# Performance work log

Hardware: AMD Instinct MI355X
Metric: run time of the kernel (lower is better)

The kernel has to match this reference:

```python
import jax, jax.numpy as jnp
import numpy as np

B, T, A, H, E = 256, 64, 32, 512, 32


def setup_inputs() -> dict:
    key = jax.random.key(0)
    ks = jax.random.split(key, 8)
    return {
        "actions": jax.random.normal(ks[0], (B, T, A), dtype=jnp.float32),
        "timesteps": jax.random.randint(ks[1], (B,), 0, 1000, dtype=jnp.int32),
        "cat_ids": jax.random.randint(ks[2], (B,), 0, E, dtype=jnp.int32),
        "W1": 0.02 * jax.random.normal(ks[3], (E, A, H), dtype=jnp.float32),
        "b1": jnp.zeros((E, H), dtype=jnp.float32),
        "W2": 0.02 * jax.random.normal(ks[4], (E, 2 * H, H), dtype=jnp.float32),
        "b2": jnp.zeros((E, H), dtype=jnp.float32),
        "W3": 0.02 * jax.random.normal(ks[5], (E, H, H), dtype=jnp.float32),
        "b3": jnp.zeros((E, H), dtype=jnp.float32),
    }


def _cat_linear(x, cat_ids, W, b):
    # per-sample weight gather + bmm, faithful to torch W[cat_ids]; bmm
    return jnp.einsum("btd,bdh->bth", x, W[cat_ids]) + b[cat_ids][:, None, :]


def _sinusoidal(timesteps_bt, dim):
    half = dim // 2
    exponent = -jnp.arange(half, dtype=jnp.float32) * (jnp.log(jnp.float32(10000.0)) / half)
    freqs = timesteps_bt[..., None] * jnp.exp(exponent)  # (B,T,half)
    return jnp.concatenate([jnp.sin(freqs), jnp.cos(freqs)], axis=-1)


def _swish(x):
    return x * jax.nn.sigmoid(x)


def reference(actions, timesteps, cat_ids, W1, b1, W2, b2, W3, b3):
    Bb, Tt, _ = actions.shape
    t_bt = jnp.broadcast_to(timesteps.astype(jnp.float32)[:, None], (Bb, Tt))
    a_emb = _cat_linear(actions, cat_ids, W1, b1)                     # (B,T,H)
    tau_emb = _sinusoidal(t_bt, a_emb.shape[-1]).astype(a_emb.dtype)  # (B,T,H)
    x = jnp.concatenate([a_emb, tau_emb], axis=-1)                    # (B,T,2H)
    x = _swish(_cat_linear(x, cat_ids, W2, b2))
    return _cat_linear(x, cat_ids, W3, b3)
```

## Files before the change

kernel.cpp:

```cpp
#include <hip/hip_runtime.h>
#include <hip/hip_bf16.h>

#define NB 256
#define NT 64
#define NA 32
#define NH 512
#define NE 32
#define MAXTILES 144

typedef short short8 __attribute__((ext_vector_type(8)));
typedef unsigned short ushort8v __attribute__((ext_vector_type(8)));
typedef float f32x4 __attribute__((ext_vector_type(4)));

__device__ __forceinline__ unsigned short f2bf(float f) {
  unsigned int u = __float_as_uint(f);
  u += 0x7FFFu + ((u >> 16) & 1u);
  return (unsigned short)(u >> 16);
}

__device__ __forceinline__ void gl2lds16(const void* g, void* l) {
  __builtin_amdgcn_global_load_lds(
      (const __attribute__((address_space(1))) unsigned int*)g,
      (__attribute__((address_space(3))) unsigned int*)l, 16, 0, 0);
}

__device__ __forceinline__ ushort8v cvt8(float4 a, float4 b) {
  ushort8v t;
  t[0] = f2bf(a.x); t[1] = f2bf(a.y); t[2] = f2bf(a.z); t[3] = f2bf(a.w);
  t[4] = f2bf(b.x); t[5] = f2bf(b.y); t[6] = f2bf(b.z); t[7] = f2bf(b.w);
  return t;
}

__device__ __forceinline__ void pfld(float2 (&pf)[8], const float* __restrict__ base,
                                     int c, int tid) {
#pragma unroll
  for (int j = 0; j < 8; j++) {
    int u = j * 256 + tid;
    int kk = u >> 7, cc = u & 127;
    pf[j] = *(const float2*)(base + (size_t)(c * 16 + kk) * NH + cc * 2);
  }
}

template <bool BIASDOT>
__device__ __forceinline__ void stream_block(
    const float* __restrict__ Wbase, float* S, unsigned short* Bs,
    const unsigned short* As, const float* b1S, int tid, int w, int lrow,
    int kq, f32x4 (&acc)[2][4], float& bacc) {
  float2 pf[2][8];
  pfld(pf[0], Wbase, 0, tid);
  pfld(pf[1], Wbase, 1, tid);
#pragma unroll 2
  for (int c = 0; c < 32; c++) {
    const int cur = c & 1;
    __syncthreads();
#pragma unroll
    for (int j = 0; j < 8; j++) {
      int u = j * 256 + tid;
      int kk = u >> 7, cc = u & 127;
      *(float2*)(&S[kk * 260 + cc * 2]) = pf[cur][j];
    }
    if (c + 2 < 32) pfld(pf[cur], Wbase, c + 2, tid);
    __syncthreads();
    {
      int n = tid;
      ushort8v pk0, pk1;
#pragma unroll
      for (int kk = 0; kk < 8; kk++) {
        float sv = S[kk * 260 + n];
        pk0[kk] = f2bf(sv);
        if (BIASDOT) bacc += sv * b1S[c * 16 + kk];
      }
#pragma unroll
      for (int kk = 8; kk < 16; kk++) {
        float sv = S[kk * 260 + n];
        pk1[kk - 8] = f2bf(sv);
        if (BIASDOT) bacc += sv * b1S[c * 16 + kk];
      }
      *(ushort8v*)(&Bs[n * 40 + cur * 16]) = pk0;
      *(ushort8v*)(&Bs[n * 40 + cur * 16 + 8]) = pk1;
    }
    if (cur) {
      __syncthreads();
      int w2i = c >> 1;
      short8 bf[4], af[2];
#pragma unroll
      for (int ni = 0; ni < 4; ni++)
        bf[ni] = *(short8*)(&Bs[(w * 64 + ni * 16 + lrow) * 40 + kq * 8]);
#pragma unroll
      for (int mi = 0; mi < 2; mi++) {
        int a = mi * 16 + lrow;
        int ck = w2i * 4 + kq;
        af[mi] = *(short8*)(&As[a * 512 + ((ck ^ (a & 7)) << 3)]);
      }
#pragma unroll
      for (int mi = 0; mi < 2; mi++)
#pragma unroll
        for (int ni = 0; ni < 4; ni++)
          acc[mi][ni] = __builtin_amdgcn_mfma_f32_16x16x32_bf16(
              af[mi], bf[ni], acc[mi][ni], 0, 0, 0);
    }
  }
}

__global__ __launch_bounds__(256) void wp2_kernel(
    const float* __restrict__ W1, const float* __restrict__ b1,
    const float* __restrict__ W2, const float* __restrict__ b2,
    const float* __restrict__ W3, const int* __restrict__ timesteps,
    const int* __restrict__ cat, unsigned short* __restrict__ Wt12,
    float* __restrict__ bias2G, float* __restrict__ tvec,
    unsigned short* __restrict__ Wt3, int* __restrict__ tiles,
    int* __restrict__ ntiles_out) {
  __shared__ __align__(16) unsigned char smem[71936];
  int tid = threadIdx.x;
  int bx = blockIdx.x;

  if (bx >= 128 && bx < 640) {
    float* S2 = (float*)smem;
    unsigned short* Bt = (unsigned short*)(smem + 33280);
    int id = bx - 128;
    int e = id >> 4, kb = (id >> 1) & 7, nh = id & 1;
    int kt = kb * 64, nt = nh * 256;
#pragma unroll
    for (int h = 0; h < 2; h++) {
      if (h) __syncthreads();
#pragma unroll
      for (int j = 0; j < 16; j++) {
        int u = j * 256 + tid;
        int kk = u >> 7, cc = u & 127;
        float2 v = *(const float2*)(W3 + ((size_t)e * 512 + kt + h * 32 + kk) * NH +
                                    nt + cc * 2);
        *(float2*)(&S2[kk * 260 + cc * 2]) = v;
      }
      __syncthreads();
      {
        int n = tid;
#pragma unroll
        for (int q = 0; q < 4; q++) {
          ushort8v pk;
#pragma unroll
          for (int jj = 0; jj < 8; jj++)
            pk[jj] = f2bf(S2[(q * 8 + jj) * 260 + n]);
          *(ushort8v*)(&Bt[n * 72 + h * 32 + q * 8]) = pk;
        }
      }
    }
    __syncthreads();
    {
      int n = tid;
      unsigned short* dst = Wt3 + (((size_t)e * 8 + kb) * 512 + nt + n) * 64;
#pragma unroll
      for (int q = 0; q < 8; q++)
        *(ushort8v*)(dst + q * 8) = *(ushort8v*)(&Bt[n * 72 + q * 8]);
    }
    return;
  }

  if (bx == 640) {
    int* cnt = (int*)smem;
    int* off = cnt + 32;
    int* cur = off + 32;
    int* order = cur + 32;
    if (tid < NE) cnt[tid] = 0;
    __syncthreads();
    int e = cat[tid];
    atomicAdd(&cnt[e], 1);
    __syncthreads();
    if (tid == 0) {
      int s = 0;
      for (int i = 0; i < NE; i++) { off[i] = s; cur[i] = s; s += cnt[i]; }
    }
    __syncthreads();
    int p = atomicAdd(&cur[e], 1);
    order[p] = tid;
    __syncthreads();
    if (tid == 0) {
      int nt = 0;
      for (int i = 0; i < NE; i++) {
        for (int j = 0; j < cnt[i]; j += 2) {
          tiles[3 * nt + 0] = i;
          tiles[3 * nt + 1] = order[off[i] + j];
          tiles[3 * nt + 2] = (j + 1 < cnt[i]) ? order[off[i] + j + 1] : -1;
          nt++;
        }
      }
      *ntiles_out = nt;
    }
    return;
  }

  float* S           = (float*)smem;
  unsigned short* Bs = (unsigned short*)(smem + 16640);
  unsigned short* As = (unsigned short*)(smem + 37120);
  float* b1S         = (float*)(smem + 69888);
  int* list          = (int*)(smem + 69888);
  int* pcnt          = (int*)(smem + 70912);

  int w = tid >> 6, l = tid & 63;
  int lrow = l & 15, kq = l >> 4;

  if (bx < 64) {
    int e = bx >> 1, nh = bx & 1;
    const float* Wbase = W2 + ((size_t)e << 19) + nh * 256;
    const float* W1e = W1 + ((size_t)e << 14);
    {
      float2 v = *(const float2*)(b1 + (size_t)e * NH + tid * 2);
      *(float2*)(&b1S[tid * 2]) = v;
    }
    {
      int a = tid >> 3, seg = tid & 7;
#pragma unroll
      for (int p = 0; p < 8; p++) {
        const float* src = W1e + (size_t)a * NH + p * 64 + seg * 8;
        float4 v0 = *(const float4*)src;
        float4 v1 = *(const float4*)(src + 4);
        int ch = p * 8 + seg;
        *(ushort8v*)(&As[a * 512 + ((ch ^ (a & 7)) << 3)]) = cvt8(v0, v1);
      }
    }
    f32x4 acc[2][4];
#pragma unroll
    for (int mi = 0; mi < 2; mi++)
#pragma unroll
      for (int ni = 0; ni < 4; ni++) acc[mi][ni] = (f32x4){0.f, 0.f, 0.f, 0.f};
    float bacc = 0.f;
    stream_block<true>(Wbase, S, Bs, As, b1S, tid, w, lrow, kq, acc, bacc);

    __syncthreads();
    unsigned short* Sb = Bs;
#pragma unroll
    for (int mi = 0; mi < 2; mi++)
#pragma unroll
      for (int ni = 0; ni < 4; ni++)
#pragma unroll
        for (int r = 0; r < 4; r++)
          Sb[(w * 64 + ni * 16 + lrow) * 40 + mi * 16 + kq * 4 + r] =
              f2bf(acc[mi][ni][r]);
    bias2G[(size_t)e * NH + nh * 256 + tid] =
        bacc + b2[(size_t)e * NH + nh * 256 + tid];
    __syncthreads();
    {
      int n = tid;
      unsigned short* dst = Wt12 + ((size_t)e * NH + nh * 256 + n) * NA;
#pragma unroll
      for (int q = 0; q < 4; q++)
        *(ushort8v*)(dst + q * 8) = *(ushort8v*)(&Sb[n * 40 + q * 8]);
    }
    return;
  }

  {
    int id = bx - 64;
    int e = id >> 1, nh = id & 1;
    const float* Wbase = W2 + ((size_t)e << 19) + ((size_t)512 * NH) + nh * 256;
    if (tid == 0) *pcnt = 0;
    __syncthreads();
    if (cat[tid] == e) { int p = atomicAdd(pcnt, 1); list[p] = tid; }
    __syncthreads();
    int c = *pcnt;
    if (c == 0) return;
    const float kLog = 0.035977893400931146f;

    for (int sg = 0; sg * 32 < c; sg++) {
      if (sg) __syncthreads();
      {
        int a = tid >> 3, seg = tid & 7;
        int si = sg * 32 + a;
        float tv = (si < c) ? (float)timesteps[list[si]] : 0.f;
#pragma unroll
        for (int p = 0; p < 8; p++) {
          ushort8v pk;
#pragma unroll
          for (int q = 0; q < 8; q++) {
            int k = p * 64 + seg * 8 + q;
            float f = expf(-(float)(k & 255) * kLog);
            float ang = tv * f;
            pk[q] = f2bf((k < 256) ? sinf(ang) : cosf(ang));
          }
          int ch = p * 8 + seg;
          *(ushort8v*)(&As[a * 512 + ((ch ^ (a & 7)) << 3)]) = pk;
        }
      }
      f32x4 acc[2][4];
#pragma unroll
      for (int mi = 0; mi < 2; mi++)
#pragma unroll
        for (int ni = 0; ni < 4; ni++) acc[mi][ni] = (f32x4){0.f, 0.f, 0.f, 0.f};
      float dummy = 0.f;
      stream_block<false>(Wbase, S, Bs, As, nullptr, tid, w, lrow, kq, acc, dummy);
#pragma unroll
      for (int mi = 0; mi < 2; mi++)
#pragma unroll
        for (int ni = 0; ni < 4; ni++)
#pragma unroll
          for (int r = 0; r < 4; r++) {
            int a = mi * 16 + kq * 4 + r;
            int si = sg * 32 + a;
            if (si < c)
              tvec[(size_t)list[si] * NH + nh * 256 + w * 64 + ni * 16 + lrow] =
                  acc[mi][ni][r];
          }
    }
  }
}

__global__ __launch_bounds__(256) void gemmh_kernel(
    const float* __restrict__ actions, const unsigned short* __restrict__ Wt12,
    const float* __restrict__ tvec, const float* __restrict__ bias2,
    const int* __restrict__ cat_ids, unsigned short* __restrict__ Hb) {
  __shared__ __align__(16) unsigned char smem[16384 + 5120 + 33792];
  unsigned short* Ws = (unsigned short*)smem;
  unsigned short* As = (unsigned short*)(smem + 16384);
  unsigned short* Ts = (unsigned short*)(smem + 16384 + 5120);

  int b = blockIdx.y, h = blockIdx.x;
  int tid = threadIdx.x;
  int e = cat_ids[b];

  {
    const unsigned short* wsrc = Wt12 + ((size_t)e * NH + h * 256) * NA;
#pragma unroll
    for (int j = 0; j < 4; j++) {
      int u = j * 256 + tid;
      int n = u >> 2, p = u & 3;
      int ch = p ^ ((n >> 1) & 3);
      gl2lds16(wsrc + (size_t)n * NA + ch * 8,
               Ws + (size_t)(j * 256 + (tid & 448)) * 8);
    }
  }
  {
    int row = tid >> 2, seg = tid & 3;
    const float* src = actions + (size_t)(b * NT + row) * NA + seg * 8;
    float4 v0 = *(const float4*)(src);
    float4 v1 = *(const float4*)(src + 4);
    *(ushort8v*)(&As[row * 40 + seg * 8]) = cvt8(v0, v1);
  }
  __syncthreads();

  int w = tid >> 6, l = tid & 63;
  int lrow = l & 15, kq = l >> 4;
  short8 af = *(short8*)(&As[(w * 16 + lrow) * 40 + kq * 8]);
  f32x4 zero = {0.f, 0.f, 0.f, 0.f};
  f32x4 acc[16];
#pragma unroll
  for (int ni = 0; ni < 16; ni++) {
    int nn = ni * 16 + lrow;
    int p = kq ^ ((nn >> 1) & 3);
    short8 bfv = *(short8*)(&Ws[nn * 32 + p * 8]);
    acc[ni] = __builtin_amdgcn_mfma_f32_16x16x32_bf16(af, bfv, zero, 0, 0, 0);
  }
#pragma unroll
  for (int ni = 0; ni < 16; ni++) {
    int colL = ni * 16 + lrow;
    float bv = tvec[(size_t)b * NH + h * 256 + colL] +
               bias2[(size_t)e * NH + h * 256 + colL];
#pragma unroll
    for (int r = 0; r < 4; r++) {
      int row = w * 16 + kq * 4 + r;
      float v = acc[ni][r] + bv;
      v = v / (1.0f + __expf(-v));
      Ts[row * 264 + colL] = f2bf(v);
    }
  }
  __syncthreads();
#pragma unroll
  for (int i = 0; i < 8; i++) {
    int u = i * 256 + tid;
    int t = u >> 5, c4 = u & 31;
    uint4 v = *(uint4*)(&Ts[t * 264 + c4 * 8]);
    *(uint4*)(Hb + ((size_t)(b * NT + t)) * NH + h * 256 + c4 * 8) = v;
  }
}

template <int KTOT, bool HASTAU, bool SWISH, bool OUT_BF16>
__global__ __launch_bounds__(256) void gemm2_kernel(
    const unsigned short* __restrict__ Xa, const unsigned short* __restrict__ Xt,
    const unsigned short* __restrict__ Wt, const float* __restrict__ bias,
    void* __restrict__ Yv, const int* __restrict__ tiles,
    const int* __restrict__ pntiles) {
  __shared__ __align__(16) unsigned char smem[49152];

  int ti = blockIdx.y;
  if (ti >= *pntiles) return;
  int n0 = blockIdx.x * 64;
  int e = tiles[3 * ti], s0 = tiles[3 * ti + 1], s1 = tiles[3 * ti + 2];
  int s1v = (s1 < 0) ? s0 : s1;

  int tid = threadIdx.x;
  int l = tid & 63;
  int wr = (tid >> 7), wc = (tid >> 6) & 1;
  int lrow = l & 15, kq = l >> 4;

  constexpr int NIT = KTOT / 64;

  auto stage = [&](int it, int buf) {
    unsigned short* As = (unsigned short*)(smem + buf * 24576);
    unsigned short* Bs = (unsigned short*)(smem + buf * 24576 + 16384);
    int k0 = it * 64;
#pragma unroll
    for (int j = 0; j < 4; j++) {
      int u = j * 256 + tid;
      int row = u >> 3, p = u & 7;
      int ch = p ^ (row & 7);
      int kk = k0 + ch * 8;
      int s = (row < 64) ? s0 : s1v;
      const unsigned short* src;
      if (HASTAU && kk >= 512)
        src = Xt + (size_t)s * NH + (kk - 512);
      else
        src = Xa + ((size_t)(s * NT + (row & 63))) * NH + kk;
      gl2lds16(src, As + (size_t)(j * 256 + (tid & 448)) * 8);
    }
#pragma unroll
    for (int j = 0; j < 2; j++) {
      int u = j * 256 + tid;
      int n = u >> 3, p = u & 7;
      int ch = p ^ (n & 7);
      gl2lds16(Wt + (((size_t)e * 8 + it) * 512 + n0 + n) * 64 + ch * 8,
               Bs + (size_t)(j * 256 + (tid & 448)) * 8);
    }
  };

  f32x4 acc[4][2];
#pragma unroll
  for (int mi = 0; mi < 4; mi++)
#pragma unroll
    for (int ni = 0; ni < 2; ni++) acc[mi][ni] = (f32x4){0.f, 0.f, 0.f, 0.f};

  stage(0, 0);
  stage(1, 1);

  for (int t = 0; t < NIT; t++) {
    int cur = t & 1;
    unsigned short* As = (unsigned short*)(smem + cur * 24576);
    unsigned short* Bs = (unsigned short*)(smem + cur * 24576 + 16384);

    if (t + 1 < NIT) {
      asm volatile("s_waitcnt vmcnt(6)" ::: "memory");
    } else {
      asm volatile("s_waitcnt vmcnt(0)" ::: "memory");
    }
    __builtin_amdgcn_sched_barrier(0);
    __builtin_amdgcn_s_barrier();
    __builtin_amdgcn_sched_barrier(0);

    short8 afr[2][4], bfr[2][2];
#pragma unroll
    for (int s2 = 0; s2 < 2; s2++) {
#pragma unroll
      for (int mi = 0; mi < 4; mi++) {
        int row = wr * 64 + mi * 16 + lrow;
        int p = (s2 * 4 + kq) ^ (row & 7);
        afr[s2][mi] = *(short8*)(&As[row * 64 + p * 8]);
      }
#pragma unroll
      for (int ni = 0; ni < 2; ni++) {
        int n = wc * 32 + ni * 16 + lrow;
        int p = (s2 * 4 + kq) ^ (n & 7);
        bfr[s2][ni] = *(short8*)(&Bs[n * 64 + p * 8]);
      }
    }
    asm volatile("s_waitcnt lgkmcnt(0)" ::: "memory");
    __builtin_amdgcn_sched_barrier(0);
    __builtin_amdgcn_s_barrier();
    __builtin_amdgcn_sched_barrier(0);

    if (t + 2 < NIT) stage(t + 2, cur);

#pragma unroll
    for (int s2 = 0; s2 < 2; s2++)
#pragma unroll
      for (int mi = 0; mi < 4; mi++)
#pragma unroll
        for (int ni = 0; ni < 2; ni++)
          acc[mi][ni] = __builtin_amdgcn_mfma_f32_16x16x32_bf16(
              afr[s2][mi], bfr[s2][ni], acc[mi][ni], 0, 0, 0);
  }
  __syncthreads();

#pragma unroll
  for (int ni = 0; ni < 2; ni++) {
    int colL = wc * 32 + ni * 16 + lrow;
    float bv = bias[(size_t)e * NH + n0 + colL];
#pragma unroll
    for (int mi = 0; mi < 4; mi++) {
#pragma unroll
      for (int r = 0; r < 4; r++) {
        int row = wr * 64 + mi * 16 + kq * 4 + r;
        float v = acc[mi][ni][r] + bv;
        if (SWISH) v = v / (1.0f + __expf(-v));
        if (OUT_BF16)
          ((unsigned short*)smem)[row * 80 + colL] = f2bf(v);
        else
          ((float*)smem)[row * 68 + colL] = v;
      }
    }
  }
  __syncthreads();
  if (OUT_BF16) {
    unsigned short* Y = (unsigned short*)Yv;
#pragma unroll
    for (int i = 0; i < 4; i++) {
      int u = i * 256 + tid;
      int row = u >> 3, c = u & 7;
      if (row >= 64 && s1 < 0) continue;
      int s = (row < 64) ? s0 : s1;
      uint4 v = *(uint4*)(&((unsigned short*)smem)[row * 80 + c * 8]);
      *(uint4*)(Y + ((size_t)(s * NT + (row & 63))) * NH + n0 + c * 8) = v;
    }
  } else {
    float* Y = (float*)Yv;
#pragma unroll
    for (int i = 0; i < 8; i++) {
      int u = i * 256 + tid;
      int row = u >> 4, c = u & 15;
      if (row >= 64 && s1 < 0) continue;
      int s = (row < 64) ? s0 : s1;
      uint4 v = *(uint4*)(&((float*)smem)[row * 68 + c * 4]);
      *(uint4*)(Y + ((size_t)(s * NT + (row & 63))) * NH + n0 + c * 4) = v;
    }
  }
}

extern "C" void kernel_launch(void* const* d_in, const int* in_sizes, int n_in,
                              void* d_out, int out_size, void* d_ws, size_t ws_size,
                              hipStream_t stream) {
  const float* actions   = (const float*)d_in[0];
  const int*   timesteps = (const int*)d_in[1];
  const int*   cat_ids   = (const int*)d_in[2];
  const float* W1 = (const float*)d_in[3];
  const float* b1 = (const float*)d_in[4];
  const float* W2 = (const float*)d_in[5];
  const float* b2 = (const float*)d_in[6];
  const float* W3 = (const float*)d_in[7];
  const float* b3 = (const float*)d_in[8];

  unsigned short* Hb   = (unsigned short*)d_ws;
  unsigned short* Wt3  = (unsigned short*)((char*)d_ws + (size_t)16777216);
  unsigned short* Wt12 = (unsigned short*)((char*)d_ws + (size_t)33554432);
  float* tvec  = (float*)((char*)d_ws + (size_t)34603008);
  float* bias2 = (float*)((char*)d_ws + (size_t)35127296);
  int* tiles   = (int*)((char*)d_ws + (size_t)35192832);
  int* ntiles  = tiles + 3 * MAXTILES;

  wp2_kernel<<<641, 256, 0, stream>>>(W1, b1, W2, b2, W3, timesteps, cat_ids,
                                      Wt12, bias2, tvec, Wt3, tiles, ntiles);
  gemmh_kernel<<<dim3(2, NB), 256, 0, stream>>>(actions, Wt12, tvec, bias2,
                                                cat_ids, Hb);
  gemm2_kernel<512, false, false, false><<<dim3(8, MAXTILES), 256, 0, stream>>>(
      Hb, nullptr, Wt3, b3, d_out, tiles, ntiles);
}
```

Measured before the change: 193.5 us.

## Split W2 preprocessing blocks into quarter-width tiles with streamed A staging

The W2-folding blocks now each cover 128 output columns instead of 256, doubling the block count to 256 and shrinking shared memory from about 72KB to 33KB. The A operand (W1 rows or sinusoidal embedding) is staged per 32-wide K chunk inside the streaming loop instead of fully up front. The W3 transpose blocks keep results in registers rather than bouncing through a second LDS buffer. The aim is more blocks per CU and better latency hiding, at the cost of extra barriers per chunk and recomputing sin/cos inside the loop.

```diff
diff --git a/kernel.cpp b/kernel.cpp
--- a/kernel.cpp
+++ b/kernel.cpp
@@ -10,6 +10,7 @@
 
 typedef short short8 __attribute__((ext_vector_type(8)));
 typedef unsigned short ushort8v __attribute__((ext_vector_type(8)));
+typedef unsigned short ushort4v __attribute__((ext_vector_type(4)));
 typedef float f32x4 __attribute__((ext_vector_type(4)));
 
 __device__ __forceinline__ unsigned short f2bf(float f) {
@@ -31,78 +32,73 @@
   return t;
 }
 
-__device__ __forceinline__ void pfld(float2 (&pf)[8], const float* __restrict__ base,
-                                     int c, int tid) {
+__device__ __forceinline__ void pfld2(float2 (&pf)[8], const float* __restrict__ base,
+                                      int c, int tid) {
 #pragma unroll
   for (int j = 0; j < 8; j++) {
     int u = j * 256 + tid;
-    int kk = u >> 7, cc = u & 127;
-    pf[j] = *(const float2*)(base + (size_t)(c * 16 + kk) * NH + cc * 2);
-  }
-}
-
-template <bool BIASDOT>
-__device__ __forceinline__ void stream_block(
+    int kk = u >> 6, cc = u & 63;
+    pf[j] = *(const float2*)(base + (size_t)(c * 32 + kk) * NH + cc * 2);
+  }
+}
+
+template <bool BIASDOT, typename AStage>
+__device__ __forceinline__ void stream2(
     const float* __restrict__ Wbase, float* S, unsigned short* Bs,
-    const unsigned short* As, const float* b1S, int tid, int w, int lrow,
-    int kq, f32x4 (&acc)[2][4], float& bacc) {
+    unsigned short* As, const float* b1S, int tid, int w, int lrow, int kq,
+    f32x4 (&acc)[2][2], float& bacc, AStage&& astage) {
   float2 pf[2][8];
-  pfld(pf[0], Wbase, 0, tid);
-  pfld(pf[1], Wbase, 1, tid);
+  pfld2(pf[0], Wbase, 0, tid);
+  pfld2(pf[1], Wbase, 1, tid);
 #pragma unroll 2
-  for (int c = 0; c < 32; c++) {
+  for (int c = 0; c < 16; c++) {
     const int cur = c & 1;
     __syncthreads();
 #pragma unroll
     for (int j = 0; j < 8; j++) {
       int u = j * 256 + tid;
-      int kk = u >> 7, cc = u & 127;
-      *(float2*)(&S[kk * 260 + cc * 2]) = pf[cur][j];
-    }
-    if (c + 2 < 32) pfld(pf[cur], Wbase, c + 2, tid);
+      int kk = u >> 6, cc = u & 63;
+      *(float2*)(&S[kk * 132 + cc * 2]) = pf[cur][j];
+    }
+    astage(c);
+    if (c + 2 < 16) pfld2(pf[cur], Wbase, c + 2, tid);
     __syncthreads();
     {
-      int n = tid;
-      ushort8v pk0, pk1;
+      int n = tid >> 1, h2 = tid & 1;
+      ushort8v p0, p1;
 #pragma unroll
       for (int kk = 0; kk < 8; kk++) {
-        float sv = S[kk * 260 + n];
-        pk0[kk] = f2bf(sv);
-        if (BIASDOT) bacc += sv * b1S[c * 16 + kk];
+        float sv = S[(h2 * 16 + kk) * 132 + n];
+        p0[kk] = f2bf(sv);
+        if (BIASDOT) bacc += sv * b1S[c * 32 + h2 * 16 + kk];
       }
 #pragma unroll
       for (int kk = 8; kk < 16; kk++) {
-        float sv = S[kk * 260 + n];
-        pk1[kk - 8] = f2bf(sv);
-        if (BIASDOT) bacc += sv * b1S[c * 16 + kk];
-      }
-      *(ushort8v*)(&Bs[n * 40 + cur * 16]) = pk0;
-      *(ushort8v*)(&Bs[n * 40 + cur * 16 + 8]) = pk1;
-    }
-    if (cur) {
-      __syncthreads();
-      int w2i = c >> 1;
-      short8 bf[4], af[2];
-#pragma unroll
-      for (int ni = 0; ni < 4; ni++)
-        bf[ni] = *(short8*)(&Bs[(w * 64 + ni * 16 + lrow) * 40 + kq * 8]);
-#pragma unroll
-      for (int mi = 0; mi < 2; mi++) {
-        int a = mi * 16 + lrow;
-        int ck = w2i * 4 + kq;
-        af[mi] = *(short8*)(&As[a * 512 + ((ck ^ (a & 7)) << 3)]);
-      }
-#pragma unroll
-      for (int mi = 0; mi < 2; mi++)
-#pragma unroll
-        for (int ni = 0; ni < 4; ni++)
-          acc[mi][ni] = __builtin_amdgcn_mfma_f32_16x16x32_bf16(
-              af[mi], bf[ni], acc[mi][ni], 0, 0, 0);
-    }
-  }
-}
-
-__global__ __launch_bounds__(256) void wp2_kernel(
+        float sv = S[(h2 * 16 + kk) * 132 + n];
+        p1[kk - 8] = f2bf(sv);
+        if (BIASDOT) bacc += sv * b1S[c * 32 + h2 * 16 + kk];
+      }
+      *(ushort8v*)(&Bs[n * 40 + h2 * 16]) = p0;
+      *(ushort8v*)(&Bs[n * 40 + h2 * 16 + 8]) = p1;
+    }
+    __syncthreads();
+    short8 bf[2], af[2];
+#pragma unroll
+    for (int ni = 0; ni < 2; ni++)
+      bf[ni] = *(short8*)(&Bs[(w * 32 + ni * 16 + lrow) * 40 + kq * 8]);
+#pragma unroll
+    for (int mi = 0; mi < 2; mi++)
+      af[mi] = *(short8*)(&As[(mi * 16 + lrow) * 40 + kq * 8]);
+#pragma unroll
+    for (int mi = 0; mi < 2; mi++)
+#pragma unroll
+      for (int ni = 0; ni < 2; ni++)
+        acc[mi][ni] = __builtin_amdgcn_mfma_f32_16x16x32_bf16(
+            af[mi], bf[ni], acc[mi][ni], 0, 0, 0);
+  }
+}
+
+__global__ __launch_bounds__(256) void wp3_kernel(
     const float* __restrict__ W1, const float* __restrict__ b1,
     const float* __restrict__ W2, const float* __restrict__ b2,
     const float* __restrict__ W3, const int* __restrict__ timesteps,
@@ -110,16 +106,16 @@
     float* __restrict__ bias2G, float* __restrict__ tvec,
     unsigned short* __restrict__ Wt3, int* __restrict__ tiles,
     int* __restrict__ ntiles_out) {
-  __shared__ __align__(16) unsigned char smem[71936];
+  __shared__ __align__(16) unsigned char smem[33280];
   int tid = threadIdx.x;
   int bx = blockIdx.x;
 
-  if (bx >= 128 && bx < 640) {
+  if (bx >= 256 && bx < 768) {
     float* S2 = (float*)smem;
-    unsigned short* Bt = (unsigned short*)(smem + 33280);
-    int id = bx - 128;
+    int id = bx - 256;
     int e = id >> 4, kb = (id >> 1) & 7, nh = id & 1;
     int kt = kb * 64, nt = nh * 256;
+    ushort8v o[8];
 #pragma unroll
     for (int h = 0; h < 2; h++) {
       if (h) __syncthreads();
@@ -140,22 +136,20 @@
 #pragma unroll
           for (int jj = 0; jj < 8; jj++)
             pk[jj] = f2bf(S2[(q * 8 + jj) * 260 + n]);
-          *(ushort8v*)(&Bt[n * 72 + h * 32 + q * 8]) = pk;
+          o[h * 4 + q] = pk;
         }
       }
     }
-    __syncthreads();
     {
       int n = tid;
       unsigned short* dst = Wt3 + (((size_t)e * 8 + kb) * 512 + nt + n) * 64;
 #pragma unroll
-      for (int q = 0; q < 8; q++)
-        *(ushort8v*)(dst + q * 8) = *(ushort8v*)(&Bt[n * 72 + q * 8]);
+      for (int q = 0; q < 8; q++) *(ushort8v*)(dst + q * 8) = o[q];
     }
     return;
   }
 
-  if (bx == 640) {
+  if (bx == 768) {
     int* cnt = (int*)smem;
     int* off = cnt + 32;
     int* cur = off + 32;
@@ -189,69 +183,76 @@
   }
 
   float* S           = (float*)smem;
-  unsigned short* Bs = (unsigned short*)(smem + 16640);
-  unsigned short* As = (unsigned short*)(smem + 37120);
-  float* b1S         = (float*)(smem + 69888);
-  int* list          = (int*)(smem + 69888);
-  int* pcnt          = (int*)(smem + 70912);
+  unsigned short* Bs = (unsigned short*)(smem + 16896);
+  unsigned short* As = (unsigned short*)(smem + 27136);
+  float* b1S         = (float*)(smem + 29696);
+  float* tauT        = (float*)(smem + 31744);
+  int* list          = (int*)(smem + 31872);
+  int* pcnt          = (int*)(smem + 32896);
 
   int w = tid >> 6, l = tid & 63;
   int lrow = l & 15, kq = l >> 4;
 
-  if (bx < 64) {
-    int e = bx >> 1, nh = bx & 1;
-    const float* Wbase = W2 + ((size_t)e << 19) + nh * 256;
+  if (bx < 128) {
+    int e = bx >> 2, nq = bx & 3;
+    const float* Wbase = W2 + ((size_t)e << 19) + nq * 128;
     const float* W1e = W1 + ((size_t)e << 14);
     {
       float2 v = *(const float2*)(b1 + (size_t)e * NH + tid * 2);
       *(float2*)(&b1S[tid * 2]) = v;
     }
+    int aa = tid >> 3, seg = tid & 7;
+    float4 pfW = *(const float4*)(W1e + (size_t)aa * NH + seg * 4);
+    f32x4 acc[2][2];
+#pragma unroll
+    for (int mi = 0; mi < 2; mi++)
+#pragma unroll
+      for (int ni = 0; ni < 2; ni++) acc[mi][ni] = (f32x4){0.f, 0.f, 0.f, 0.f};
+    float bacc = 0.f;
+
+    stream2<true>(Wbase, S, Bs, As, b1S, tid, w, lrow, kq, acc, bacc,
+                  [&](int c) {
+                    ushort4v pk;
+                    pk[0] = f2bf(pfW.x); pk[1] = f2bf(pfW.y);
+                    pk[2] = f2bf(pfW.z); pk[3] = f2bf(pfW.w);
+                    *(ushort4v*)(&As[aa * 40 + seg * 4]) = pk;
+                    if (c + 1 < 16)
+                      pfW = *(const float4*)(W1e + (size_t)aa * NH +
+                                             (c + 1) * 32 + seg * 4);
+                  });
+
+    __syncthreads();
+    unsigned short* Sb = Bs;
+#pragma unroll
+    for (int mi = 0; mi < 2; mi++)
+#pragma unroll
+      for (int ni = 0; ni < 2; ni++)
+#pragma unroll
+        for (int r = 0; r < 4; r++)
+          Sb[(w * 32 + ni * 16 + lrow) * 40 + mi * 16 + kq * 4 + r] =
+              f2bf(acc[mi][ni][r]);
     {
-      int a = tid >> 3, seg = tid & 7;
-#pragma unroll
-      for (int p = 0; p < 8; p++) {
-        const float* src = W1e + (size_t)a * NH + p * 64 + seg * 8;
-        float4 v0 = *(const float4*)src;
-        float4 v1 = *(const float4*)(src + 4);
-        int ch = p * 8 + seg;
-        *(ushort8v*)(&As[a * 512 + ((ch ^ (a & 7)) << 3)]) = cvt8(v0, v1);
-      }
-    }
-    f32x4 acc[2][4];
-#pragma unroll
-    for (int mi = 0; mi < 2; mi++)
-#pragma unroll
-      for (int ni = 0; ni < 4; ni++) acc[mi][ni] = (f32x4){0.f, 0.f, 0.f, 0.f};
-    float bacc = 0.f;
-    stream_block<true>(Wbase, S, Bs, As, b1S, tid, w, lrow, kq, acc, bacc);
-
-    __syncthreads();
-    unsigned short* Sb = Bs;
-#pragma unroll
-    for (int mi = 0; mi < 2; mi++)
-#pragma unroll
-      for (int ni = 0; ni < 4; ni++)
-#pragma unroll
-        for (int r = 0; r < 4; r++)
-          Sb[(w * 64 + ni * 16 + lrow) * 40 + mi * 16 + kq * 4 + r] =
-              f2bf(acc[mi][ni][r]);
-    bias2G[(size_t)e * NH + nh * 256 + tid] =
-        bacc + b2[(size_t)e * NH + nh * 256 + tid];
+      float bsum = bacc + __shfl_xor(bacc, 1);
+      if ((tid & 1) == 0) {
+        int n = tid >> 1;
+        bias2G[(size_t)e * NH + nq * 128 + n] =
+            bsum + b2[(size_t)e * NH + nq * 128 + n];
+      }
+    }
     __syncthreads();
     {
-      int n = tid;
-      unsigned short* dst = Wt12 + ((size_t)e * NH + nh * 256 + n) * NA;
-#pragma unroll
-      for (int q = 0; q < 4; q++)
-        *(ushort8v*)(dst + q * 8) = *(ushort8v*)(&Sb[n * 40 + q * 8]);
+      int n = tid >> 1, q = tid & 1;
+      unsigned short* dst = Wt12 + ((size_t)e * NH + nq * 128 + n) * NA + q * 16;
+      *(ushort8v*)(dst) = *(ushort8v*)(&Sb[n * 40 + q * 16]);
+      *(ushort8v*)(dst + 8) = *(ushort8v*)(&Sb[n * 40 + q * 16 + 8]);
     }
     return;
   }
 
   {
-    int id = bx - 64;
-    int e = id >> 1, nh = id & 1;
-    const float* Wbase = W2 + ((size_t)e << 19) + ((size_t)512 * NH) + nh * 256;
+    int id = bx - 128;
+    int e = id >> 2, nq = id & 3;
+    const float* Wbase = W2 + ((size_t)e << 19) + ((size_t)512 * NH) + nq * 128;
     if (tid == 0) *pcnt = 0;
     __syncthreads();
     if (cat[tid] == e) { int p = atomicAdd(pcnt, 1); list[p] = tid; }
@@ -259,46 +260,45 @@
     int c = *pcnt;
     if (c == 0) return;
     const float kLog = 0.035977893400931146f;
+    int ss = tid >> 3, seg = tid & 7;
 
     for (int sg = 0; sg * 32 < c; sg++) {
-      if (sg) __syncthreads();
-      {
-        int a = tid >> 3, seg = tid & 7;
-        int si = sg * 32 + a;
-        float tv = (si < c) ? (float)timesteps[list[si]] : 0.f;
-#pragma unroll
-        for (int p = 0; p < 8; p++) {
-          ushort8v pk;
-#pragma unroll
-          for (int q = 0; q < 8; q++) {
-            int k = p * 64 + seg * 8 + q;
-            float f = expf(-(float)(k & 255) * kLog);
-            float ang = tv * f;
-            pk[q] = f2bf((k < 256) ? sinf(ang) : cosf(ang));
-          }
-          int ch = p * 8 + seg;
-          *(ushort8v*)(&As[a * 512 + ((ch ^ (a & 7)) << 3)]) = pk;
-        }
-      }
-      f32x4 acc[2][4];
+      if (tid < 32) {
+        int si = sg * 32 + tid;
+        tauT[tid] = (si < c) ? (float)timesteps[list[si]] : 0.f;
+      }
+      f32x4 acc[2][2];
 #pragma unroll
       for (int mi = 0; mi < 2; mi++)
 #pragma unroll
-        for (int ni = 0; ni < 4; ni++) acc[mi][ni] = (f32x4){0.f, 0.f, 0.f, 0.f};
+        for (int ni = 0; ni < 2; ni++) acc[mi][ni] = (f32x4){0.f, 0.f, 0.f, 0.f};
       float dummy = 0.f;
-      stream_block<false>(Wbase, S, Bs, As, nullptr, tid, w, lrow, kq, acc, dummy);
+
+      stream2<false>(Wbase, S, Bs, As, nullptr, tid, w, lrow, kq, acc, dummy,
+                     [&](int cch) {
+                       float tv = tauT[ss];
+                       ushort4v pk;
+#pragma unroll
+                       for (int q = 0; q < 4; q++) {
+                         int kg = cch * 32 + seg * 4 + q;
+                         float f = expf(-(float)(kg & 255) * kLog);
+                         float ang = tv * f;
+                         pk[q] = f2bf((kg < 256) ? sinf(ang) : cosf(ang));
+                       }
+                       *(ushort4v*)(&As[ss * 40 + seg * 4]) = pk;
+                     });
 #pragma unroll
       for (int mi = 0; mi < 2; mi++)
 #pragma unroll
-        for (int ni = 0; ni < 4; ni++)
+        for (int ni = 0; ni < 2; ni++)
 #pragma unroll
           for (int r = 0; r < 4; r++) {
-            int a = mi * 16 + kq * 4 + r;
-            int si = sg * 32 + a;
+            int si = sg * 32 + mi * 16 + kq * 4 + r;
             if (si < c)
-              tvec[(size_t)list[si] * NH + nh * 256 + w * 64 + ni * 16 + lrow] =
+              tvec[(size_t)list[si] * NH + nq * 128 + w * 32 + ni * 16 + lrow] =
                   acc[mi][ni][r];
           }
+      __syncthreads();
     }
   }
 }
@@ -542,7 +542,7 @@
   int* tiles   = (int*)((char*)d_ws + (size_t)35192832);
   int* ntiles  = tiles + 3 * MAXTILES;
 
-  wp2_kernel<<<641, 256, 0, stream>>>(W1, b1, W2, b2, W3, timesteps, cat_ids,
+  wp3_kernel<<<769, 256, 0, stream>>>(W1, b1, W2, b2, W3, timesteps, cat_ids,
                                       Wt12, bias2, tvec, Wt3, tiles, ntiles);
   gemmh_kernel<<<dim3(2, NB), 256, 0, stream>>>(actions, Wt12, tvec, bias2,
                                                 cat_ids, Hb);
```

New measurement: 188.4 us. 1.03x faster.
